# Performance work log

Measured on AMD Instinct MI355X. Metric: run time of the kernel, lower is better.

## Reference

```python
import jax, jax.numpy as jnp
import numpy as np

B, H_WIN, W_WIN = 2048, 8, 8
N = H_WIN * W_WIN            # tokens per window = 64
C = 384                      # channels
HEADS, HEAD_DIM = 12, 32
E = HEADS * HEAD_DIM         # embedding channels = 384
EPS = 1e-5


def _relative_position_indices(h, w):
    coords = np.stack(np.meshgrid(np.arange(h), np.arange(w), indexing='ij')).reshape(2, -1)  # [2, N]
    rel = coords[:, :, None] - coords[:, None, :]      # [2, N, N]
    rel = rel.transpose(1, 2, 0).astype(np.int64)      # [N, N, 2]
    rel[..., 0] = (rel[..., 0] + h - 1) * (2 * w - 1)
    rel[..., 1] += w - 1
    return rel.sum(-1)                                 # [N, N] in [0, (2h-1)(2w-1))


def setup_inputs() -> dict:
    key = jax.random.key(0)
    ks = jax.random.split(key, 6)
    x = jax.random.normal(ks[0], (B, N, C), dtype=jnp.float32)
    ln_g = jnp.ones((C,), jnp.float32)
    ln_b = jnp.zeros((C,), jnp.float32)
    w_qkv = jax.random.normal(ks[1], (3 * E, C), jnp.float32) * (1.0 / np.sqrt(C))
    w_out = jax.random.normal(ks[2], (C, E), jnp.float32) * (1.0 / np.sqrt(E))
    b_out = jnp.zeros((C,), jnp.float32)
    n_bias = (2 * H_WIN - 1) * (2 * W_WIN - 1)
    bias_table = jax.random.truncated_normal(ks[3], -2.0, 2.0, (n_bias, HEADS), jnp.float32) * 0.02
    rel_idx = jnp.asarray(_relative_position_indices(H_WIN, W_WIN))  # [N, N] int64
    return {"x": x, "ln_g": ln_g, "ln_b": ln_b, "w_qkv": w_qkv,
            "w_out": w_out, "b_out": b_out, "bias_table": bias_table, "rel_idx": rel_idx}


def reference(x, ln_g, ln_b, w_qkv, w_out, b_out, bias_table, rel_idx):
    # pre-norm
    mu = jnp.mean(x, axis=-1, keepdims=True)
    var = jnp.var(x, axis=-1, keepdims=True)
    xn = (x - mu) * jax.lax.rsqrt(var + EPS) * ln_g + ln_b
    # qkv projection (no bias)
    qkv = jnp.einsum('bnc,ec->bne', xn, w_qkv)                     # [B, N, 3E]
    qkv = qkv.reshape(x.shape[0], N, 3, HEADS, HEAD_DIM)
    q, k, v = (qkv[:, :, i].transpose(0, 2, 1, 3) for i in range(3))  # each [B, h, N, d]
    scale = 1.0 / np.sqrt(HEAD_DIM)
    scores = jnp.einsum('bhnd,bhmd->bhnm', q * scale, k)           # [B, h, N, N]
    # gather learned relative-position bias per (n, m) pair
    bias = bias_table[rel_idx]                                     # [N, N, h]
    scores = scores + bias.transpose(2, 0, 1)[None]                # broadcast over B
    p = jax.nn.softmax(scores, axis=-1)
    out = jnp.einsum('bhnm,bhmd->bhnd', p, v)                      # [B, h, N, d]
    out = out.transpose(0, 2, 1, 3).reshape(x.shape[0], N, E)
    return jnp.einsum('bne,ce->bnc', out, w_out) + b_out
```

## Files before the change

### kernel.cpp

```cpp
#include <hip/hip_runtime.h>
#include <hip/hip_bf16.h>


#define NTOK  64
#define CCH   384
#define NH    12
#define HD    32
#define EPSV  1e-5f
#define SCALEQ 0.17677669529663687f

#define WQP_ELEMS (72 * 12 * 64 * 8)
#define WOP_ELEMS (24 * 12 * 64 * 8)
#define BLUTP_ELEMS (12 * 4 * 4 * 64 * 4)

typedef __attribute__((ext_vector_type(8))) short  short8;
typedef __attribute__((ext_vector_type(4))) short  short4v;
typedef __attribute__((ext_vector_type(4))) float  float4v;
typedef __attribute__((ext_vector_type(4))) int    int4v;

__device__ __forceinline__ unsigned short f2bf(float f) {
    union { float f; unsigned int i; } v; v.f = f;
    unsigned int r = v.i + 0x7fffu + ((v.i >> 16) & 1u);
    return (unsigned short)(r >> 16);
}
__device__ __forceinline__ unsigned int pack2bf(float lo, float hi) {
    return (unsigned int)f2bf(lo) | ((unsigned int)f2bf(hi) << 16);
}

__global__ void prep_kernel(const float* __restrict__ w_qkv_f,
                            const float* __restrict__ w_out_f,
                            const float* __restrict__ bias_tab,
                            const int*   __restrict__ rel_idx,
                            unsigned short* __restrict__ wqp,
                            unsigned short* __restrict__ wop,
                            float* __restrict__ blutp) {
    const int stride = gridDim.x * blockDim.x;
    const int tid = blockIdx.x * blockDim.x + threadIdx.x;
    for (int i = tid; i < WQP_ELEMS; i += stride) {
        const int t = i / 6144, rem = i % 6144;
        const int kk = rem >> 9, rem2 = rem & 511;
        const int lane = rem2 >> 3, e = rem2 & 7;
        wqp[i] = f2bf(w_qkv_f[(16 * t + (lane & 15)) * CCH + 32 * kk + 8 * (lane >> 4) + e]);
    }
    for (int i = tid; i < WOP_ELEMS; i += stride) {
        const int t = i / 6144, rem = i % 6144;
        const int kk = rem >> 9, rem2 = rem & 511;
        const int lane = rem2 >> 3, e = rem2 & 7;
        wop[i] = f2bf(w_out_f[(16 * t + (lane & 15)) * CCH + 32 * kk + 8 * (lane >> 4) + e]);
    }
    for (int i = tid; i < BLUTP_ELEMS; i += stride) {
        const int r = i & 3, lane = (i >> 2) & 63;
        const int kt = (i >> 8) & 3, tt = (i >> 10) & 3, h = i >> 12;
        const int token = 16 * tt + (lane & 15);
        const int key   = 16 * kt + 4 * (lane >> 4) + r;
        blutp[i] = bias_tab[rel_idx[token * 64 + key] * NH + h];
    }
}

__global__ __launch_bounds__(512, 2)
void fused_win_mha(const float* __restrict__ x,
                   const float* __restrict__ ln_g,
                   const float* __restrict__ ln_b,
                   const float* __restrict__ b_out,
                   const unsigned short* __restrict__ wqp,
                   const unsigned short* __restrict__ wop,
                   const float* __restrict__ blutp,
                   float* __restrict__ out)
{
    const int b    = blockIdx.x;
    const int t    = threadIdx.x;
    const int wav  = t >> 6;
    const int lane = t & 63;
    const int l4   = lane >> 4;
    const int lc   = lane & 15;
    const int lh   = wav >> 1;
    const int mh   = wav & 1;

    __shared__ unsigned short xnp[4 * 12 * 64 * 8];
    __shared__ unsigned short qp [4 * 4 * 64 * 8];
    __shared__ unsigned short kp [4 * 4 * 64 * 8];
    __shared__ unsigned short vp [2][4 * 2 * 2 * 64 * 8];
    __shared__ unsigned short attp[4 * 4 * 64 * 8];

    {
        const int row = t >> 3, seg = t & 7;
        const float* xr = x + (b * NTOK + row) * CCH + seg * 48;
        float vals[48];
        float s = 0.f, s2 = 0.f;
        #pragma unroll
        for (int i = 0; i < 12; ++i) {
            float4v v = *(const float4v*)(xr + i * 4);
            #pragma unroll
            for (int j = 0; j < 4; ++j) {
                float f = v[j];
                vals[i * 4 + j] = f; s += f; s2 += f * f;
            }
        }
        s += __shfl_xor(s, 1); s2 += __shfl_xor(s2, 1);
        s += __shfl_xor(s, 2); s2 += __shfl_xor(s2, 2);
        s += __shfl_xor(s, 4); s2 += __shfl_xor(s2, 4);
        const float mu   = s * (1.f / CCH);
        const float rstd = rsqrtf(s2 * (1.f / CCH) - mu * mu + EPSV);
        #pragma unroll
        for (int u = 0; u < 6; ++u) {
            const int col0 = seg * 48 + u * 8;
            short8 w;
            #pragma unroll
            for (int e2 = 0; e2 < 2; ++e2) {
                float4v gv = *(const float4v*)(ln_g + col0 + e2 * 4);
                float4v bv = *(const float4v*)(ln_b + col0 + e2 * 4);
                #pragma unroll
                for (int j = 0; j < 4; ++j)
                    w[e2 * 4 + j] = (short)f2bf((vals[u * 8 + e2 * 4 + j] - mu) * rstd * gv[j] + bv[j]);
            }
            const int idx = ((((row >> 4) * 12 + (col0 >> 5)) << 9)
                             + ((((col0 >> 3) & 3) * 16 + (row & 15)) << 3));
            *(short8*)&xnp[idx] = w;
        }
    }
    __syncthreads();

    float4v facc[4][3];
    #pragma unroll
    for (int mt = 0; mt < 4; ++mt)
        #pragma unroll
        for (int j = 0; j < 3; ++j)
            facc[mt][j] = (float4v){0.f, 0.f, 0.f, 0.f};

    float sv[2][4][4];
    float mx[2];
    float4v bbn[2][4];

    #pragma unroll
    for (int it = 0; it < 4; ++it) {
        if (it < 3) {
            const int h = 4 * it + lh;
            #pragma unroll
            for (int j = 0; j < 2; ++j)
                #pragma unroll
                for (int kt = 0; kt < 4; ++kt)
                    bbn[j][kt] = *(const float4v*)(blutp + ((((h * 4 + (2 * mh + j)) * 4 + kt) << 6) + lane) * 4);
        }

        short8 af[2][2];
        if (it > 0) {
            unsigned int pk2[2][4][2];
            #pragma unroll
            for (int j = 0; j < 2; ++j) {
                float sk[4];
                #pragma unroll
                for (int kt = 0; kt < 4; ++kt) {
                    float pe0 = __expf(sv[j][kt][0] - mx[j]);
                    float pe1 = __expf(sv[j][kt][1] - mx[j]);
                    float pe2 = __expf(sv[j][kt][2] - mx[j]);
                    float pe3 = __expf(sv[j][kt][3] - mx[j]);
                    sv[j][kt][0] = pe0; sv[j][kt][1] = pe1;
                    sv[j][kt][2] = pe2; sv[j][kt][3] = pe3;
                    sk[kt] = (pe0 + pe1) + (pe2 + pe3);
                }
                float s = (sk[0] + sk[1]) + (sk[2] + sk[3]);
                s += __shfl_xor(s, 16);
                s += __shfl_xor(s, 32);
                const float rinv = 1.f / s;
                #pragma unroll
                for (int kt = 0; kt < 4; ++kt) {
                    pk2[j][kt][0] = pack2bf(sv[j][kt][0] * rinv, sv[j][kt][1] * rinv);
                    pk2[j][kt][1] = pack2bf(sv[j][kt][2] * rinv, sv[j][kt][3] * rinv);
                }
            }
            const int src0 = lc + 16 * (2 * (l4 & 1));
            const int src1 = src0 + 16;
            const bool hi  = ((l4 >> 1) & 1) != 0;
            #pragma unroll
            for (int j = 0; j < 2; ++j) {
                #pragma unroll
                for (int kk2 = 0; kk2 < 2; ++kk2) {
                    const int ka = 2 * kk2, kb = 2 * kk2 + 1;
                    unsigned int a0a = (unsigned int)__shfl((int)pk2[j][ka][0], src0);
                    unsigned int a0b = (unsigned int)__shfl((int)pk2[j][kb][0], src0);
                    unsigned int a1a = (unsigned int)__shfl((int)pk2[j][ka][1], src0);
                    unsigned int a1b = (unsigned int)__shfl((int)pk2[j][kb][1], src0);
                    unsigned int a2a = (unsigned int)__shfl((int)pk2[j][ka][0], src1);
                    unsigned int a2b = (unsigned int)__shfl((int)pk2[j][kb][0], src1);
                    unsigned int a3a = (unsigned int)__shfl((int)pk2[j][ka][1], src1);
                    unsigned int a3b = (unsigned int)__shfl((int)pk2[j][kb][1], src1);
                    int4v iv;
                    iv[0] = (int)(hi ? a0b : a0a);
                    iv[1] = (int)(hi ? a1b : a1a);
                    iv[2] = (int)(hi ? a2b : a2a);
                    iv[3] = (int)(hi ? a3b : a3a);
                    af[j][kk2] = __builtin_bit_cast(short8, iv);
                }
            }
        }

        float4v acc[3][4];
        int tile_[3];
        if (it < 3) {
            const int h = 4 * it + lh;
            #pragma unroll
            for (int n = 0; n < 3; ++n) {
                tile_[n] = n * 24 + h * 2 + mh;
                #pragma unroll
                for (int m = 0; m < 4; ++m)
                    acc[n][m] = (float4v){0.f, 0.f, 0.f, 0.f};
            }
            #pragma unroll
            for (int kk = 0; kk < 12; ++kk) {
                short8 aF[4];
                #pragma unroll
                for (int mt = 0; mt < 4; ++mt)
                    aF[mt] = *(const short8*)&xnp[((mt * 12 + kk) << 9) + (lane << 3)];
                short8 bF0 = *(const short8*)&wqp[((tile_[0] * 12 + kk) << 9) + (lane << 3)];
                short8 bF1 = *(const short8*)&wqp[((tile_[1] * 12 + kk) << 9) + (lane << 3)];
                short8 bF2 = *(const short8*)&wqp[((tile_[2] * 12 + kk) << 9) + (lane << 3)];
                #pragma unroll
                for (int mt = 0; mt < 4; ++mt) {
                    acc[0][mt] = __builtin_amdgcn_mfma_f32_16x16x32_bf16(bF0, aF[mt], acc[0][mt], 0, 0, 0);
                    acc[1][mt] = __builtin_amdgcn_mfma_f32_16x16x32_bf16(bF1, aF[mt], acc[1][mt], 0, 0, 0);
                    acc[2][mt] = __builtin_amdgcn_mfma_f32_16x16x32_bf16(aF[mt], bF2, acc[2][mt], 0, 0, 0);
                }
            }
        }

        if (it > 0) {
            const unsigned short* vpr = vp[(it - 1) & 1];
            float4v o[2][2];
            #pragma unroll
            for (int j = 0; j < 2; ++j)
                #pragma unroll
                for (int nt = 0; nt < 2; ++nt)
                    o[j][nt] = (float4v){0.f, 0.f, 0.f, 0.f};
            #pragma unroll
            for (int kk2 = 0; kk2 < 2; ++kk2) {
                #pragma unroll
                for (int nt = 0; nt < 2; ++nt) {
                    short8 vf = *(const short8*)&vpr[(((lh * 2 + nt) * 2 + kk2) << 9) + (lane << 3)];
                    #pragma unroll
                    for (int j = 0; j < 2; ++j)
                        o[j][nt] = __builtin_amdgcn_mfma_f32_16x16x32_bf16(vf, af[j][kk2], o[j][nt], 0, 0, 0);
                }
            }
            #pragma unroll
            for (int j = 0; j < 2; ++j) {
                #pragma unroll
                for (int nt = 0; nt < 2; ++nt) {
                    short4v pa;
                    #pragma unroll
                    for (int r = 0; r < 4; ++r)
                        pa[r] = (short)f2bf(o[j][nt][r]);
                    const int addr = (((2 * mh + j) * 4 + lh) << 9)
                                   + (((2 * nt + (l4 >> 1)) * 16 + lc) << 3)
                                   + ((l4 & 1) << 2);
                    *(short4v*)&attp[addr] = pa;
                }
            }
        }

        if (it < 3) {
            unsigned short* vpw = vp[it & 1];
            #pragma unroll
            for (int mt = 0; mt < 4; ++mt) {
                short4v pq, pkk, pv;
                #pragma unroll
                for (int r = 0; r < 4; ++r) {
                    pq[r]  = (short)f2bf(acc[0][mt][r] * SCALEQ);
                    pkk[r] = (short)f2bf(acc[1][mt][r]);
                    pv[r]  = (short)f2bf(acc[2][mt][r]);
                }
                const int aqk = ((lh * 4 + mt) << 9)
                              + (((2 * mh + (l4 >> 1)) * 16 + lc) << 3)
                              + ((l4 & 1) << 2);
                *(short4v*)&qp[aqk] = pq;
                *(short4v*)&kp[aqk] = pkk;
                const int av = (((lh * 2 + mh) * 2 + (mt >> 1)) << 9)
                             + ((((mt & 1) * 2 + (l4 >> 1)) * 16 + lc) << 3)
                             + ((l4 & 1) << 2);
                *(short4v*)&vpw[av] = pv;
            }
        }
        __syncthreads();

        if (it > 0) {
            const int g = it - 1;
            #pragma unroll
            for (int ks = 0; ks < 4; ++ks) {
                short8 aG[4];
                #pragma unroll
                for (int mt = 0; mt < 4; ++mt)
                    aG[mt] = *(const short8*)&attp[((mt * 4 + ks) << 9) + (lane << 3)];
                #pragma unroll
                for (int j2 = 0; j2 < 3; ++j2) {
                    short8 bG = *(const short8*)&wop[(((3 * wav + j2) * 12 + 4 * g + ks) << 9) + (lane << 3)];
                    #pragma unroll
                    for (int mt = 0; mt < 4; ++mt)
                        facc[mt][j2] = __builtin_amdgcn_mfma_f32_16x16x32_bf16(aG[mt], bG, facc[mt][j2], 0, 0, 0);
                }
            }
        }
        if (it < 3) {
            #pragma unroll
            for (int j = 0; j < 2; ++j) {
                short8 qf = *(const short8*)&qp[((lh * 4 + (2 * mh + j)) << 9) + (lane << 3)];
                #pragma unroll
                for (int kt = 0; kt < 4; ++kt) {
                    short8 kf = *(const short8*)&kp[((lh * 4 + kt) << 9) + (lane << 3)];
                    float4v sres = __builtin_amdgcn_mfma_f32_16x16x32_bf16(
                        kf, qf, (float4v){0.f, 0.f, 0.f, 0.f}, 0, 0, 0);
                    #pragma unroll
                    for (int r = 0; r < 4; ++r) sv[j][kt][r] = sres[r];
                }
            }
            #pragma unroll
            for (int j = 0; j < 2; ++j) {
                float m = -1e30f;
                #pragma unroll
                for (int kt = 0; kt < 4; ++kt) {
                    #pragma unroll
                    for (int r = 0; r < 4; ++r) {
                        sv[j][kt][r] += bbn[j][kt][r];
                        m = fmaxf(m, sv[j][kt][r]);
                    }
                }
                m = fmaxf(m, __shfl_xor(m, 16));
                m = fmaxf(m, __shfl_xor(m, 32));
                mx[j] = m;
            }
        }
        __syncthreads();
    }

    {
        float* ob = out + b * (NTOK * CCH);
        #pragma unroll
        for (int mt = 0; mt < 4; ++mt) {
            #pragma unroll
            for (int j2 = 0; j2 < 3; ++j2) {
                const int c = 16 * (3 * wav + j2) + lc;
                const float bo = b_out[c];
                #pragma unroll
                for (int r = 0; r < 4; ++r)
                    ob[(16 * mt + 4 * l4 + r) * CCH + c] = facc[mt][j2][r] + bo;
            }
        }
    }
}

extern "C" void kernel_launch(void* const* d_in, const int* in_sizes, int n_in,
                              void* d_out, int out_size, void* d_ws, size_t ws_size,
                              hipStream_t stream) {
    const float* x     = (const float*)d_in[0];
    const float* ln_g  = (const float*)d_in[1];
    const float* ln_b  = (const float*)d_in[2];
    const float* w_qkv = (const float*)d_in[3];
    const float* w_out = (const float*)d_in[4];
    const float* b_out = (const float*)d_in[5];
    const float* btab  = (const float*)d_in[6];
    const int*   ridx  = (const int*)d_in[7];
    float*       out   = (float*)d_out;

    unsigned short* wqp   = (unsigned short*)d_ws;
    unsigned short* wop   = wqp + WQP_ELEMS;
    float*          blutp = (float*)(wop + WOP_ELEMS);

    prep_kernel<<<512, 256, 0, stream>>>(w_qkv, w_out, btab, ridx, wqp, wop, blutp);
    fused_win_mha<<<2048, 512, 0, stream>>>(x, ln_g, ln_b, b_out, wqp, wop, blutp, out);
}
```

Measured before the change: 285.4 us.

## Re-tile QKV and output projections per wave to halve shared-memory fragment loads

Changes the per-wave work split in the QKV projection and the output projection. Each wave now covers two row tiles (selected by mh) and six column tiles, instead of all four row tiles and three column tiles. This lowers LDS fragment reads per MFMA: per k-step a wave loads 2 A plus 6 B fragments for 12 MFMAs, where it used to load 4 A plus 3 B. The Q/K/V write-back and output store indexing are remapped to match, and K fragments in the score loop are hoisted so they are loaded once rather than per j. The new wave-to-column mapping changes global weight-load patterns, and the wider B-fragment arrays may raise register pressure.

```diff
diff --git a/kernel.cpp b/kernel.cpp
--- a/kernel.cpp
+++ b/kernel.cpp
@@ -25,6 +25,12 @@
 }
 __device__ __forceinline__ unsigned int pack2bf(float lo, float hi) {
     return (unsigned int)f2bf(lo) | ((unsigned int)f2bf(hi) << 16);
+}
+__device__ __forceinline__ short4v pack4bf(float a, float b, float c, float d) {
+    short4v p;
+    p[0] = (short)f2bf(a); p[1] = (short)f2bf(b);
+    p[2] = (short)f2bf(c); p[3] = (short)f2bf(d);
+    return p;
 }
 
 __global__ void prep_kernel(const float* __restrict__ w_qkv_f,
@@ -120,12 +126,12 @@
     }
     __syncthreads();
 
-    float4v facc[4][3];
+    float4v facc[2][6];
     #pragma unroll
-    for (int mt = 0; mt < 4; ++mt)
+    for (int mtl = 0; mtl < 2; ++mtl)
         #pragma unroll
-        for (int j = 0; j < 3; ++j)
-            facc[mt][j] = (float4v){0.f, 0.f, 0.f, 0.f};
+        for (int j = 0; j < 6; ++j)
+            facc[mtl][j] = (float4v){0.f, 0.f, 0.f, 0.f};
 
     float sv[2][4][4];
     float mx[2];
@@ -194,31 +200,34 @@
             }
         }
 
-        float4v acc[3][4];
-        int tile_[3];
+        float4v acc[6][2];
+        int tile_[6];
         if (it < 3) {
             const int h = 4 * it + lh;
             #pragma unroll
-            for (int n = 0; n < 3; ++n) {
-                tile_[n] = n * 24 + h * 2 + mh;
-                #pragma unroll
-                for (int m = 0; m < 4; ++m)
-                    acc[n][m] = (float4v){0.f, 0.f, 0.f, 0.f};
+            for (int s = 0; s < 6; ++s) {
+                tile_[s] = (s >> 1) * 24 + h * 2 + (s & 1);
+                acc[s][0] = (float4v){0.f, 0.f, 0.f, 0.f};
+                acc[s][1] = (float4v){0.f, 0.f, 0.f, 0.f};
             }
             #pragma unroll
             for (int kk = 0; kk < 12; ++kk) {
-                short8 aF[4];
-                #pragma unroll
-                for (int mt = 0; mt < 4; ++mt)
-                    aF[mt] = *(const short8*)&xnp[((mt * 12 + kk) << 9) + (lane << 3)];
-                short8 bF0 = *(const short8*)&wqp[((tile_[0] * 12 + kk) << 9) + (lane << 3)];
-                short8 bF1 = *(const short8*)&wqp[((tile_[1] * 12 + kk) << 9) + (lane << 3)];
-                short8 bF2 = *(const short8*)&wqp[((tile_[2] * 12 + kk) << 9) + (lane << 3)];
-                #pragma unroll
-                for (int mt = 0; mt < 4; ++mt) {
-                    acc[0][mt] = __builtin_amdgcn_mfma_f32_16x16x32_bf16(bF0, aF[mt], acc[0][mt], 0, 0, 0);
-                    acc[1][mt] = __builtin_amdgcn_mfma_f32_16x16x32_bf16(bF1, aF[mt], acc[1][mt], 0, 0, 0);
-                    acc[2][mt] = __builtin_amdgcn_mfma_f32_16x16x32_bf16(aF[mt], bF2, acc[2][mt], 0, 0, 0);
+                short8 aF[2];
+                #pragma unroll
+                for (int mtl = 0; mtl < 2; ++mtl)
+                    aF[mtl] = *(const short8*)&xnp[(((2 * mh + mtl) * 12 + kk) << 9) + (lane << 3)];
+                short8 bF[6];
+                #pragma unroll
+                for (int s = 0; s < 6; ++s)
+                    bF[s] = *(const short8*)&wqp[((tile_[s] * 12 + kk) << 9) + (lane << 3)];
+                #pragma unroll
+                for (int mtl = 0; mtl < 2; ++mtl) {
+                    acc[0][mtl] = __builtin_amdgcn_mfma_f32_16x16x32_bf16(bF[0], aF[mtl], acc[0][mtl], 0, 0, 0);
+                    acc[1][mtl] = __builtin_amdgcn_mfma_f32_16x16x32_bf16(bF[1], aF[mtl], acc[1][mtl], 0, 0, 0);
+                    acc[2][mtl] = __builtin_amdgcn_mfma_f32_16x16x32_bf16(bF[2], aF[mtl], acc[2][mtl], 0, 0, 0);
+                    acc[3][mtl] = __builtin_amdgcn_mfma_f32_16x16x32_bf16(bF[3], aF[mtl], acc[3][mtl], 0, 0, 0);
+                    acc[4][mtl] = __builtin_amdgcn_mfma_f32_16x16x32_bf16(aF[mtl], bF[4], acc[4][mtl], 0, 0, 0);
+                    acc[5][mtl] = __builtin_amdgcn_mfma_f32_16x16x32_bf16(aF[mtl], bF[5], acc[5][mtl], 0, 0, 0);
                 }
             }
         }
@@ -245,14 +254,10 @@
             for (int j = 0; j < 2; ++j) {
                 #pragma unroll
                 for (int nt = 0; nt < 2; ++nt) {
-                    short4v pa;
-                    #pragma unroll
-                    for (int r = 0; r < 4; ++r)
-                        pa[r] = (short)f2bf(o[j][nt][r]);
                     const int addr = (((2 * mh + j) * 4 + lh) << 9)
                                    + (((2 * nt + (l4 >> 1)) * 16 + lc) << 3)
                                    + ((l4 & 1) << 2);
-                    *(short4v*)&attp[addr] = pa;
+                    *(short4v*)&attp[addr] = pack4bf(o[j][nt][0], o[j][nt][1], o[j][nt][2], o[j][nt][3]);
                 }
             }
         }
@@ -260,23 +265,23 @@
         if (it < 3) {
             unsigned short* vpw = vp[it & 1];
             #pragma unroll
-            for (int mt = 0; mt < 4; ++mt) {
-                short4v pq, pkk, pv;
-                #pragma unroll
-                for (int r = 0; r < 4; ++r) {
-                    pq[r]  = (short)f2bf(acc[0][mt][r] * SCALEQ);
-                    pkk[r] = (short)f2bf(acc[1][mt][r]);
-                    pv[r]  = (short)f2bf(acc[2][mt][r]);
-                }
-                const int aqk = ((lh * 4 + mt) << 9)
-                              + (((2 * mh + (l4 >> 1)) * 16 + lc) << 3)
-                              + ((l4 & 1) << 2);
-                *(short4v*)&qp[aqk] = pq;
-                *(short4v*)&kp[aqk] = pkk;
-                const int av = (((lh * 2 + mh) * 2 + (mt >> 1)) << 9)
-                             + ((((mt & 1) * 2 + (l4 >> 1)) * 16 + lc) << 3)
-                             + ((l4 & 1) << 2);
-                *(short4v*)&vpw[av] = pv;
+            for (int mtl = 0; mtl < 2; ++mtl) {
+                const int mt = 2 * mh + mtl;
+                #pragma unroll
+                for (int half = 0; half < 2; ++half) {
+                    const int aqk = ((lh * 4 + mt) << 9)
+                                  + (((2 * half + (l4 >> 1)) * 16 + lc) << 3)
+                                  + ((l4 & 1) << 2);
+                    *(short4v*)&qp[aqk] = pack4bf(acc[half][mtl][0] * SCALEQ, acc[half][mtl][1] * SCALEQ,
+                                                  acc[half][mtl][2] * SCALEQ, acc[half][mtl][3] * SCALEQ);
+                    *(short4v*)&kp[aqk] = pack4bf(acc[2 + half][mtl][0], acc[2 + half][mtl][1],
+                                                  acc[2 + half][mtl][2], acc[2 + half][mtl][3]);
+                    const int av = (((lh * 2 + half) * 2 + mh) << 9)
+                                 + (((mtl * 2 + (l4 >> 1)) * 16 + lc) << 3)
+                                 + ((l4 & 1) << 2);
+                    *(short4v*)&vpw[av] = pack4bf(acc[4 + half][mtl][0], acc[4 + half][mtl][1],
+                                                  acc[4 + half][mtl][2], acc[4 + half][mtl][3]);
+                }
             }
         }
         __syncthreads();
@@ -285,28 +290,31 @@
             const int g = it - 1;
             #pragma unroll
             for (int ks = 0; ks < 4; ++ks) {
-                short8 aG[4];
-                #pragma unroll
-                for (int mt = 0; mt < 4; ++mt)
-                    aG[mt] = *(const short8*)&attp[((mt * 4 + ks) << 9) + (lane << 3)];
-                #pragma unroll
-                for (int j2 = 0; j2 < 3; ++j2) {
-                    short8 bG = *(const short8*)&wop[(((3 * wav + j2) * 12 + 4 * g + ks) << 9) + (lane << 3)];
+                short8 aG[2];
+                #pragma unroll
+                for (int mtl = 0; mtl < 2; ++mtl)
+                    aG[mtl] = *(const short8*)&attp[(((2 * mh + mtl) * 4 + ks) << 9) + (lane << 3)];
+                #pragma unroll
+                for (int j2 = 0; j2 < 6; ++j2) {
+                    short8 bG = *(const short8*)&wop[(((6 * lh + j2) * 12 + 4 * g + ks) << 9) + (lane << 3)];
                     #pragma unroll
-                    for (int mt = 0; mt < 4; ++mt)
-                        facc[mt][j2] = __builtin_amdgcn_mfma_f32_16x16x32_bf16(aG[mt], bG, facc[mt][j2], 0, 0, 0);
+                    for (int mtl = 0; mtl < 2; ++mtl)
+                        facc[mtl][j2] = __builtin_amdgcn_mfma_f32_16x16x32_bf16(aG[mtl], bG, facc[mtl][j2], 0, 0, 0);
                 }
             }
         }
         if (it < 3) {
+            short8 kf[4];
+            #pragma unroll
+            for (int kt = 0; kt < 4; ++kt)
+                kf[kt] = *(const short8*)&kp[((lh * 4 + kt) << 9) + (lane << 3)];
             #pragma unroll
             for (int j = 0; j < 2; ++j) {
                 short8 qf = *(const short8*)&qp[((lh * 4 + (2 * mh + j)) << 9) + (lane << 3)];
                 #pragma unroll
                 for (int kt = 0; kt < 4; ++kt) {
-                    short8 kf = *(const short8*)&kp[((lh * 4 + kt) << 9) + (lane << 3)];
                     float4v sres = __builtin_amdgcn_mfma_f32_16x16x32_bf16(
-                        kf, qf, (float4v){0.f, 0.f, 0.f, 0.f}, 0, 0, 0);
+                        kf[kt], qf, (float4v){0.f, 0.f, 0.f, 0.f}, 0, 0, 0);
                     #pragma unroll
                     for (int r = 0; r < 4; ++r) sv[j][kt][r] = sres[r];
                 }
@@ -333,14 +341,14 @@
     {
         float* ob = out + b * (NTOK * CCH);
         #pragma unroll
-        for (int mt = 0; mt < 4; ++mt) {
-            #pragma unroll
-            for (int j2 = 0; j2 < 3; ++j2) {
-                const int c = 16 * (3 * wav + j2) + lc;
+        for (int mtl = 0; mtl < 2; ++mtl) {
+            #pragma unroll
+            for (int j2 = 0; j2 < 6; ++j2) {
+                const int c = 16 * (6 * lh + j2) + lc;
                 const float bo = b_out[c];
                 #pragma unroll
                 for (int r = 0; r < 4; ++r)
-                    ob[(16 * mt + 4 * l4 + r) * CCH + c] = facc[mt][j2][r] + bo;
+                    ob[(16 * (2 * mh + mtl) + 4 * l4 + r) * CCH + c] = facc[mtl][j2][r] + bo;
             }
         }
     }
```

New measurement: 323.6 us. 1.13x slower.
